# Optimization experiments

Hardware: AMD Instinct MI355X
Metric: run time of the kernel (lower is better)

Reference implementation:

```python
import math
import jax, jax.numpy as jnp
import numpy as np

B, T, HIDDEN = 2, 2048, 1024
H, HKV, D = 16, 16, 64


def _rope_tables(T, D):
    inv_freq = 1.0 / (10000.0 ** (jnp.arange(0, D, 2, dtype=jnp.float32) / D))
    t = jnp.arange(T, dtype=jnp.float32)
    freqs = jnp.outer(t, inv_freq)               # [T, D/2]
    emb = jnp.concatenate([freqs, freqs], axis=-1)  # [T, D]
    return jnp.cos(emb), jnp.sin(emb)


def setup_inputs() -> dict:
    key = jax.random.key(0)
    k1, k2, k3 = jax.random.split(key, 3)
    hidden_states = jax.random.normal(k1, (B, T, HIDDEN), dtype=jnp.float32)
    cos, sin = _rope_tables(T, D)
    # trunc-normal-ish init, std = 1/sqrt(fan_in)
    w_qkv = jax.random.normal(k2, ((H + 2 * HKV) * D, HIDDEN), dtype=jnp.float32) / math.sqrt(HIDDEN)
    w_o = jax.random.normal(k3, (HIDDEN, H * D), dtype=jnp.float32) / math.sqrt(H * D)
    return {"hidden_states": hidden_states, "cos": cos, "sin": sin, "w_qkv": w_qkv, "w_o": w_o}


def _rotate_half(x):
    x1, x2 = jnp.split(x, 2, axis=-1)
    return jnp.concatenate([-x2, x1], axis=-1)


def reference(hidden_states, cos, sin, w_qkv, w_o):
    b, t, _ = hidden_states.shape
    # fused QKV projection: [B,T,(H+2*HKV)*D]
    qkv = jnp.einsum('bti,oi->bto', hidden_states, w_qkv)
    qkv = qkv.reshape(b, t, H + 2 * HKV, D)
    q = qkv[:, :, :H]                    # [B,T,H,D]
    k = qkv[:, :, H:H + HKV]             # [B,T,HKV,D]
    v = qkv[:, :, H + HKV:]              # [B,T,HKV,D]
    # inline RoPE; cos/sin broadcast over heads
    c = cos[:, None, :]
    s = sin[:, None, :]
    q = q * c + _rotate_half(q) * s
    k = k * c + _rotate_half(k) * s
    scale = 1.0 / math.sqrt(D)
    attn_scores = jnp.einsum('bthd,bThd->bhtT', q, k) * scale  # [B,H,T,T]
    mask = jnp.tril(jnp.ones((t, t), dtype=bool))
    attn_scores = jnp.where(mask[None, None, :, :], attn_scores, -1e9)
    attn = jax.nn.softmax(attn_scores, axis=-1)
    context = jnp.einsum('bhtT,bThd->bthd', attn, v).reshape(b, t, H * D)
    return jnp.einsum('bti,oi->bto', context, w_o)
```

## Files before the change

kernel.cpp:

```cpp
#include <hip/hip_runtime.h>

typedef __bf16 bf16_t;
typedef __bf16 bf16x4 __attribute__((ext_vector_type(4)));
typedef __bf16 bf16x8 __attribute__((ext_vector_type(8)));
typedef float f32x4 __attribute__((ext_vector_type(4)));
typedef unsigned int u32x2 __attribute__((ext_vector_type(2)));
typedef unsigned long long u64;

#define MFMA16(a, b, c) __builtin_amdgcn_mfma_f32_16x16x32_bf16((a), (b), (c), 0, 0, 0)

#define LDG2LDS16(g, l)                                                        \
    __builtin_amdgcn_global_load_lds(                                          \
        (const __attribute__((address_space(1))) void*)(g),                    \
        (__attribute__((address_space(3))) void*)(l), 16, 0, 0)

#if __has_builtin(__builtin_amdgcn_exp2f)
#define EXP2(x) __builtin_amdgcn_exp2f(x)
#else
#define EXP2(x) exp2f(x)
#endif

__device__ inline bf16x8 load8(const float* p) {
    const f32x4 a = *(const f32x4*)p;
    const f32x4 b = *(const f32x4*)(p + 4);
    bf16x8 r;
#pragma unroll
    for (int i = 0; i < 4; i++) { r[i] = (bf16_t)a[i]; r[4 + i] = (bf16_t)b[i]; }
    return r;
}

__device__ inline u32x2 as2(bf16x4 v) {
    u32x2 r;
    __builtin_memcpy(&r, &v, 8);
    return r;
}

__device__ inline bf16x4 shfl4(bf16x4 v, int src) {
    u64 x;
    __builtin_memcpy(&x, &v, 8);
    x = __shfl(x, src, 64);
    bf16x4 r;
    __builtin_memcpy(&r, &x, 8);
    return r;
}

__global__ __launch_bounds__(256) void convert_kernel(const float* __restrict__ hs,
                                                      const float* __restrict__ wqkv,
                                                      const float* __restrict__ wo,
                                                      bf16_t* __restrict__ outb) {
    const size_t c = ((size_t)blockIdx.x * 256 + threadIdx.x) * 8;
    const float* src;
    size_t off;
    if (c < 4194304) { src = hs; off = c; }
    else if (c < 7340032) { src = wqkv; off = c - 4194304; }
    else { src = wo; off = c - 7340032; }
    *(bf16x8*)(outb + c) = load8(src + off);
}


template <int MODE, int NDIM, int BM>
__global__ __launch_bounds__(256) void gemm_bt(const bf16_t* __restrict__ A,
                                               const bf16_t* __restrict__ B,
                                               float* __restrict__ outp,
                                               bf16_t* __restrict__ q_ws,
                                               bf16_t* __restrict__ k_ws,
                                               bf16_t* __restrict__ v_ws,
                                               const float* __restrict__ cosb,
                                               const float* __restrict__ sinb) {
    constexpr int K = 1024;
    constexpr int IM = BM / 32;
    __shared__ __align__(16) bf16_t As[BM * 32];
    __shared__ __align__(16) bf16_t Bs[128 * 32];

    const int tid = threadIdx.x;
    const int w = tid >> 6;
    const int lane = tid & 63;
    const int lr = lane & 15;
    const int quad = lane >> 4;
    const int m0 = blockIdx.y * BM;
    const int n0 = blockIdx.x * 128;
    const int wm = (w & 1) * (BM / 2);
    const int wn = (w >> 1) * 64;

    const int srow = tid >> 2;
    const int skk = (((tid & 3) ^ ((tid >> 3) & 3)) * 8);
    const bf16_t* gA0 = A + (size_t)(m0 + srow) * K + skk;
    const bf16_t* gA1 = gA0 + (size_t)64 * K;
    const bf16_t* gB0 = B + (size_t)(n0 + srow) * K + skk;
    const bf16_t* gB1 = gB0 + (size_t)64 * K;
    bf16_t* lA0 = As + w * 512;
    bf16_t* lA1 = As + 2048 + w * 512;
    bf16_t* lB0 = Bs + w * 512;
    bf16_t* lB1 = Bs + 2048 + w * 512;

    const int qsw = (quad ^ ((lr >> 1) & 3)) * 8;

    f32x4 acc[IM][4] = {};

    for (int k0 = 0; k0 < K; k0 += 32) {
        LDG2LDS16(gA0 + k0, lA0);
        if constexpr (BM == 128) LDG2LDS16(gA1 + k0, lA1);
        LDG2LDS16(gB0 + k0, lB0);
        LDG2LDS16(gB1 + k0, lB1);
        __syncthreads();

        bf16x8 af[IM], bfm[4];
#pragma unroll
        for (int im = 0; im < IM; im++)
            af[im] = *(const bf16x8*)&As[(wm + im * 16 + lr) * 32 + qsw];
#pragma unroll
        for (int in = 0; in < 4; in++)
            bfm[in] = *(const bf16x8*)&Bs[(wn + in * 16 + lr) * 32 + qsw];
#pragma unroll
        for (int im = 0; im < IM; im++)
#pragma unroll
            for (int in = 0; in < 4; in++)
                acc[im][in] = MFMA16(af[im], bfm[in], acc[im][in]);
        __syncthreads();
    }

    if constexpr (MODE == 0) {
#pragma unroll
        for (int im = 0; im < IM; im++)
#pragma unroll
            for (int in = 0; in < 4; in++)
#pragma unroll
                for (int r = 0; r < 4; r++) {
                    const int m = m0 + wm + im * 16 + quad * 4 + r;
                    const int n = n0 + wn + in * 16 + lr;
                    outp[(size_t)m * NDIM + n] = acc[im][in][r];
                }
    } else {
        const int j = (n0 + wn) >> 6;
        if (j < 32) {
            const bool isq = (j < 16);
            const float qs = 0.125f * 1.44269504089f;
#pragma unroll
            for (int im = 0; im < IM; im++) {
#pragma unroll
                for (int r = 0; r < 4; r++) {
                    const int m = m0 + wm + im * 16 + quad * 4 + r;
                    const int b = m >> 11;
                    const int t = m & 2047;
#pragma unroll
                    for (int in = 0; in < 2; in++) {
                        const int d = in * 16 + lr;
                        const float x1 = acc[im][in][r];
                        const float x2 = acc[im][in + 2][r];
                        const float c = cosb[t * 64 + d];
                        const float s = sinb[t * 64 + d];
                        float y1 = x1 * c - x2 * s;
                        float y2 = x2 * c + x1 * s;
                        if (isq) {
                            y1 *= qs; y2 *= qs;
                            const size_t base =
                                ((size_t)(b * 16 + j) * 2048 + t) * 64 + d;
                            q_ws[base] = (bf16_t)y1;
                            q_ws[base + 32] = (bf16_t)y2;
                        } else {
                            const int bh = b * 16 + (j - 16);
                            const size_t off =
                                ((size_t)(bh * 128 + (t >> 4)) * 2) * 512 +
                                ((t & 15) + (d >> 3) * 16) * 8 + (d & 7);
                            k_ws[off] = (bf16_t)y1;
                            k_ws[off + 512] = (bf16_t)y2;
                        }
                    }
                }
            }
        } else {
#pragma unroll
            for (int im = 0; im < IM; im++)
#pragma unroll
                for (int in = 0; in < 4; in++)
#pragma unroll
                    for (int r = 0; r < 4; r++) {
                        const int m = m0 + wm + im * 16 + quad * 4 + r;
                        const int b = m >> 11;
                        const int t = m & 2047;
                        const int d = in * 16 + lr;
                        const int bh = b * 16 + (j - 32);
                        const size_t off =
                            ((size_t)(bh * 64 + (t >> 5)) * 4 + (d >> 4)) * 512 +
                            ((d & 15) + ((t & 31) >> 3) * 16) * 8 + (t & 7);
                        v_ws[off] = (bf16_t)acc[im][in][r];
                    }
        }
    }
}

__global__ __launch_bounds__(256) void attn_kernel(const bf16_t* __restrict__ q_ws,
                                                   const bf16_t* __restrict__ k_ws,
                                                   const bf16_t* __restrict__ v_ws,
                                                   bf16_t* __restrict__ ctx) {
    __shared__ __align__(16) bf16_t Ks[2][4096];
    __shared__ __align__(16) bf16_t Vs[2][4096];

    const int tid = threadIdx.x;
    const int w = tid >> 6;
    const int lane = tid & 63;
    const int lr = lane & 15;
    const int quad = lane >> 4;
    const int bh = blockIdx.x & 31;
    const int g = blockIdx.x >> 5;
    const int qt = (g & 1) ? (g >> 1) : (31 - (g >> 1));
    const int b = bh >> 4;
    const int hd = bh & 15;

    const bf16_t* kws = k_ws + (size_t)bh * 131072;
    const bf16_t* vws = v_ws + (size_t)bh * 131072;
    const int soff = w * 512 + lane * 8;
    const int lo8 = lane * 8;

#define ASTAGE(kb, buf)                                                        \
    {                                                                          \
        LDG2LDS16(kws + (size_t)(kb) * 4096 + soff, &Ks[buf][w * 512]);        \
        LDG2LDS16(kws + (size_t)(kb) * 4096 + 2048 + soff,                     \
                  &Ks[buf][2048 + w * 512]);                                   \
        LDG2LDS16(vws + (size_t)(kb) * 4096 + soff, &Vs[buf][w * 512]);        \
        LDG2LDS16(vws + (size_t)(kb) * 4096 + 2048 + soff,                     \
                  &Vs[buf][2048 + w * 512]);                                   \
    }

    const int trow = qt * 64 + w * 16;
    const int query = trow + lr;

    const bf16_t* qb = q_ws + ((size_t)bh * 2048 + trow + lr) * 64 + quad * 8;
    const bf16x8 qlo = *(const bf16x8*)qb;
    const bf16x8 qhi = *(const bf16x8*)(qb + 32);

    f32x4 o[4] = {};
    float lrun = 0.0f;

    ASTAGE(0, 0);
    asm volatile("s_waitcnt vmcnt(0)" ::: "memory");
    __builtin_amdgcn_s_barrier();
    asm volatile("" ::: "memory");

    for (int kb = 0; kb <= qt; kb++) {
        const int buf = kb & 1;
        if (kb < qt) ASTAGE(kb + 1, buf ^ 1);

        f32x4 s[4];
#pragma unroll
        for (int n = 0; n < 4; n++) {
            const bf16x8 k0 = *(const bf16x8*)&Ks[buf][(2 * n) * 512 + lo8];
            const bf16x8 k1 = *(const bf16x8*)&Ks[buf][(2 * n + 1) * 512 + lo8];
            const f32x4 z = {};
            s[n] = MFMA16(k0, qlo, z);
            s[n] = MFMA16(k1, qhi, s[n]);
        }

        const int u0 = kb * 64;
        if (kb == qt) {
#pragma unroll
            for (int n = 0; n < 4; n++)
#pragma unroll
                for (int r = 0; r < 4; r++)
                    if (u0 + n * 16 + quad * 4 + r > query) s[n][r] = -1e9f;
        }

        f32x4 p[4];
#pragma unroll
        for (int n = 0; n < 4; n++)
#pragma unroll
            for (int r = 0; r < 4; r++) p[n][r] = EXP2(s[n][r]);

        lrun += ((p[0][0] + p[0][1]) + (p[0][2] + p[0][3])) +
                ((p[1][0] + p[1][1]) + (p[1][2] + p[1][3])) +
                ((p[2][0] + p[2][1]) + (p[2][2] + p[2][3])) +
                ((p[3][0] + p[3][1]) + (p[3][2] + p[3][3]));

        bf16x4 pb[4];
#pragma unroll
        for (int n = 0; n < 4; n++)
#pragma unroll
            for (int r = 0; r < 4; r++) pb[n][r] = (bf16_t)p[n][r];

#pragma unroll
        for (int hh = 0; hh < 2; hh++) {
            bf16x8 pf;
#if __has_builtin(__builtin_amdgcn_permlane16_swap) && \
    __has_builtin(__builtin_amdgcn_permlane32_swap)
            const u32x2 P0 = as2(pb[2 * hh]);
            const u32x2 P1 = as2(pb[2 * hh + 1]);
            const u32x2 s1a = __builtin_amdgcn_permlane16_swap(P0[0], P0[1], false, false);
            const u32x2 s1b = __builtin_amdgcn_permlane16_swap(P1[0], P1[1], false, false);
            const u32x2 s2a = __builtin_amdgcn_permlane32_swap(s1a[0], s1b[0], false, false);
            const u32x2 s2b = __builtin_amdgcn_permlane32_swap(s1a[1], s1b[1], false, false);
            const u32x2 s3a = __builtin_amdgcn_permlane16_swap(s2a[0], s2a[1], false, false);
            const u32x2 s3b = __builtin_amdgcn_permlane16_swap(s2b[0], s2b[1], false, false);
            const unsigned pfd[4] = {s3a[0], s3a[1], s3b[0], s3b[1]};
            __builtin_memcpy(&pf, pfd, 16);
#else
            const int srcLow = ((quad & 1) << 5) + lr;
            const int srcHigh = srcLow + 16;
            const bool loSel = (quad < 2);
            const bf16x4 a0 = shfl4(pb[2 * hh], srcLow);
            const bf16x4 a1 = shfl4(pb[2 * hh + 1], srcLow);
            const bf16x4 b0 = shfl4(pb[2 * hh], srcHigh);
            const bf16x4 b1 = shfl4(pb[2 * hh + 1], srcHigh);
            const bf16x4 lo = loSel ? a0 : a1;
            const bf16x4 hi = loSel ? b0 : b1;
#pragma unroll
            for (int r = 0; r < 4; r++) { pf[r] = lo[r]; pf[4 + r] = hi[r]; }
#endif
#pragma unroll
            for (int n = 0; n < 4; n++) {
                const bf16x8 vvf =
                    *(const bf16x8*)&Vs[buf][(hh * 4 + n) * 512 + lo8];
                o[n] = MFMA16(vvf, pf, o[n]);
            }
        }

        asm volatile("s_waitcnt lgkmcnt(0) vmcnt(0)" ::: "memory");
        __builtin_amdgcn_s_barrier();
        asm volatile("" ::: "memory");
    }

    lrun += __shfl_xor(lrun, 16);
    lrun += __shfl_xor(lrun, 32);

    const float inv = 1.0f / fmaxf(lrun, 1e-30f);
    const size_t base = ((size_t)b * 2048 + query) * 1024 + hd * 64 + quad * 4;
#pragma unroll
    for (int n = 0; n < 4; n++) {
        bf16x4 ob;
#pragma unroll
        for (int r = 0; r < 4; r++) ob[r] = (bf16_t)(o[n][r] * inv);
        *(bf16x4*)&ctx[base + n * 16] = ob;
    }
#undef ASTAGE
}

extern "C" void kernel_launch(void* const* d_in, const int* in_sizes, int n_in,
                              void* d_out, int out_size, void* d_ws, size_t ws_size,
                              hipStream_t stream) {
    const float* hs = (const float*)d_in[0];
    const float* cosb = (const float*)d_in[1];
    const float* sinb = (const float*)d_in[2];
    const float* wqkv = (const float*)d_in[3];
    const float* wo = (const float*)d_in[4];
    float* out = (float*)d_out;

    char* ws = (char*)d_ws;
    bf16_t* hs_b = (bf16_t*)(ws);
    bf16_t* wqkv_b = hs_b + 4194304;
    bf16_t* wo_b = hs_b + 7340032;
    bf16_t* q_ws = (bf16_t*)(ws + (size_t)(16u << 20));
    bf16_t* k_ws = (bf16_t*)(ws + (size_t)(24u << 20));
    bf16_t* v_ws = (bf16_t*)(ws + (size_t)(32u << 20));
    bf16_t* ctx = (bf16_t*)(ws);

    const dim3 blk(256);

    convert_kernel<<<dim3(4096), blk, 0, stream>>>(hs, wqkv, wo, hs_b);

    gemm_bt<1, 3072, 128><<<dim3(24, 32), blk, 0, stream>>>(
        hs_b, wqkv_b, nullptr, q_ws, k_ws, v_ws, cosb, sinb);

    attn_kernel<<<dim3(1024), blk, 0, stream>>>(q_ws, k_ws, v_ws, ctx);

    gemm_bt<0, 1024, 64><<<dim3(8, 64), blk, 0, stream>>>(
        ctx, wo_b, out, nullptr, nullptr, nullptr, nullptr, nullptr);
}
```

Before: 176.1 us.

## Pair causal query tiles per 512-thread block and compute row sums via MFMA

The attention kernel now uses 512-thread blocks, each handling two query tiles (qt and 31-qt), so every block does the same total causal work and shares the K/V LDS stages. The first four waves stage K and the other four stage V. The softmax row-sum is moved from scalar adds plus cross-lane shuffles to an extra MFMA against a ones vector, and exp values go straight to bf16. Waves on the short tile sit idle at barriers once their rows are done, and the denominator is now summed from bf16-rounded probabilities.

```diff
diff --git a/kernel.cpp b/kernel.cpp
--- a/kernel.cpp
+++ b/kernel.cpp
@@ -42,6 +42,36 @@
     bf16x4 r;
     __builtin_memcpy(&r, &x, 8);
     return r;
+}
+
+__device__ inline bf16x8 p2pf(bf16x4 pb0, bf16x4 pb1, int quad, int lr) {
+    bf16x8 pf;
+#if __has_builtin(__builtin_amdgcn_permlane16_swap) && \
+    __has_builtin(__builtin_amdgcn_permlane32_swap)
+    const u32x2 P0 = as2(pb0);
+    const u32x2 P1 = as2(pb1);
+    const u32x2 s1a = __builtin_amdgcn_permlane16_swap(P0[0], P0[1], false, false);
+    const u32x2 s1b = __builtin_amdgcn_permlane16_swap(P1[0], P1[1], false, false);
+    const u32x2 s2a = __builtin_amdgcn_permlane32_swap(s1a[0], s1b[0], false, false);
+    const u32x2 s2b = __builtin_amdgcn_permlane32_swap(s1a[1], s1b[1], false, false);
+    const u32x2 s3a = __builtin_amdgcn_permlane16_swap(s2a[0], s2a[1], false, false);
+    const u32x2 s3b = __builtin_amdgcn_permlane16_swap(s2b[0], s2b[1], false, false);
+    const unsigned pfd[4] = {s3a[0], s3a[1], s3b[0], s3b[1]};
+    __builtin_memcpy(&pf, pfd, 16);
+#else
+    const int srcLow = ((quad & 1) << 5) + lr;
+    const int srcHigh = srcLow + 16;
+    const bool loSel = (quad < 2);
+    const bf16x4 a0 = shfl4(pb0, srcLow);
+    const bf16x4 a1 = shfl4(pb1, srcLow);
+    const bf16x4 b0 = shfl4(pb0, srcHigh);
+    const bf16x4 b1 = shfl4(pb1, srcHigh);
+    const bf16x4 lo = loSel ? a0 : a1;
+    const bf16x4 hi = loSel ? b0 : b1;
+#pragma unroll
+    for (int r = 0; r < 4; r++) { pf[r] = lo[r]; pf[4 + r] = hi[r]; }
+#endif
+    return pf;
 }
 
 __global__ __launch_bounds__(256) void convert_kernel(const float* __restrict__ hs,
@@ -189,40 +219,51 @@
     }
 }
 
-__global__ __launch_bounds__(256) void attn_kernel(const bf16_t* __restrict__ q_ws,
-                                                   const bf16_t* __restrict__ k_ws,
-                                                   const bf16_t* __restrict__ v_ws,
-                                                   bf16_t* __restrict__ ctx) {
+__global__ __launch_bounds__(512, 4) void attn_kernel(const bf16_t* __restrict__ q_ws,
+                                                      const bf16_t* __restrict__ k_ws,
+                                                      const bf16_t* __restrict__ v_ws,
+                                                      bf16_t* __restrict__ ctx) {
     __shared__ __align__(16) bf16_t Ks[2][4096];
     __shared__ __align__(16) bf16_t Vs[2][4096];
 
     const int tid = threadIdx.x;
     const int w = tid >> 6;
+    const int wq = w & 3;
     const int lane = tid & 63;
     const int lr = lane & 15;
     const int quad = lane >> 4;
     const int bh = blockIdx.x & 31;
     const int g = blockIdx.x >> 5;
-    const int qt = (g & 1) ? (g >> 1) : (31 - (g >> 1));
+    const int pr = (g < 8) ? g : 23 - g;
+    const int qtA = pr;
+    const int qtB = 31 - pr;
+    const int qtw = (w < 4) ? qtA : qtB;
     const int b = bh >> 4;
     const int hd = bh & 15;
 
     const bf16_t* kws = k_ws + (size_t)bh * 131072;
     const bf16_t* vws = v_ws + (size_t)bh * 131072;
-    const int soff = w * 512 + lane * 8;
+    const int soff = wq * 512 + lane * 8;
     const int lo8 = lane * 8;
 
-#define ASTAGE(kb, buf)                                                        \
+    bf16x8 ones8;
+#pragma unroll
+    for (int i = 0; i < 8; i++) ones8[i] = (bf16_t)1.0f;
+
+#define ASTAGE(kb, bufi)                                                       \
     {                                                                          \
-        LDG2LDS16(kws + (size_t)(kb) * 4096 + soff, &Ks[buf][w * 512]);        \
-        LDG2LDS16(kws + (size_t)(kb) * 4096 + 2048 + soff,                     \
-                  &Ks[buf][2048 + w * 512]);                                   \
-        LDG2LDS16(vws + (size_t)(kb) * 4096 + soff, &Vs[buf][w * 512]);        \
-        LDG2LDS16(vws + (size_t)(kb) * 4096 + 2048 + soff,                     \
-                  &Vs[buf][2048 + w * 512]);                                   \
-    }
-
-    const int trow = qt * 64 + w * 16;
+        if (w < 4) {                                                           \
+            LDG2LDS16(kws + (size_t)(kb) * 4096 + soff, &Ks[bufi][wq * 512]);  \
+            LDG2LDS16(kws + (size_t)(kb) * 4096 + 2048 + soff,                 \
+                      &Ks[bufi][2048 + wq * 512]);                             \
+        } else {                                                               \
+            LDG2LDS16(vws + (size_t)(kb) * 4096 + soff, &Vs[bufi][wq * 512]);  \
+            LDG2LDS16(vws + (size_t)(kb) * 4096 + 2048 + soff,                 \
+                      &Vs[bufi][2048 + wq * 512]);                             \
+        }                                                                      \
+    }
+
+    const int trow = qtw * 64 + wq * 16;
     const int query = trow + lr;
 
     const bf16_t* qb = q_ws + ((size_t)bh * 2048 + trow + lr) * 64 + quad * 8;
@@ -230,86 +271,54 @@
     const bf16x8 qhi = *(const bf16x8*)(qb + 32);
 
     f32x4 o[4] = {};
-    float lrun = 0.0f;
+    f32x4 lacc = {};
 
     ASTAGE(0, 0);
     asm volatile("s_waitcnt vmcnt(0)" ::: "memory");
     __builtin_amdgcn_s_barrier();
     asm volatile("" ::: "memory");
 
-    for (int kb = 0; kb <= qt; kb++) {
-        const int buf = kb & 1;
-        if (kb < qt) ASTAGE(kb + 1, buf ^ 1);
-
-        f32x4 s[4];
-#pragma unroll
-        for (int n = 0; n < 4; n++) {
-            const bf16x8 k0 = *(const bf16x8*)&Ks[buf][(2 * n) * 512 + lo8];
-            const bf16x8 k1 = *(const bf16x8*)&Ks[buf][(2 * n + 1) * 512 + lo8];
-            const f32x4 z = {};
-            s[n] = MFMA16(k0, qlo, z);
-            s[n] = MFMA16(k1, qhi, s[n]);
-        }
-
-        const int u0 = kb * 64;
-        if (kb == qt) {
+    for (int kb = 0; kb <= qtB; kb++) {
+        const int bufi = kb & 1;
+        if (kb < qtB) ASTAGE(kb + 1, bufi ^ 1);
+
+        if (kb <= qtw) {
+            f32x4 s[4];
+#pragma unroll
+            for (int n = 0; n < 4; n++) {
+                const bf16x8 k0 = *(const bf16x8*)&Ks[bufi][(2 * n) * 512 + lo8];
+                const bf16x8 k1 =
+                    *(const bf16x8*)&Ks[bufi][(2 * n + 1) * 512 + lo8];
+                const f32x4 z = {};
+                s[n] = MFMA16(k0, qlo, z);
+                s[n] = MFMA16(k1, qhi, s[n]);
+            }
+
+            const int u0 = kb * 64;
+            if (kb == qtw) {
+#pragma unroll
+                for (int n = 0; n < 4; n++)
+#pragma unroll
+                    for (int r = 0; r < 4; r++)
+                        if (u0 + n * 16 + quad * 4 + r > query) s[n][r] = -1e9f;
+            }
+
+            bf16x4 pb[4];
 #pragma unroll
             for (int n = 0; n < 4; n++)
 #pragma unroll
-                for (int r = 0; r < 4; r++)
-                    if (u0 + n * 16 + quad * 4 + r > query) s[n][r] = -1e9f;
-        }
-
-        f32x4 p[4];
-#pragma unroll
-        for (int n = 0; n < 4; n++)
-#pragma unroll
-            for (int r = 0; r < 4; r++) p[n][r] = EXP2(s[n][r]);
-
-        lrun += ((p[0][0] + p[0][1]) + (p[0][2] + p[0][3])) +
-                ((p[1][0] + p[1][1]) + (p[1][2] + p[1][3])) +
-                ((p[2][0] + p[2][1]) + (p[2][2] + p[2][3])) +
-                ((p[3][0] + p[3][1]) + (p[3][2] + p[3][3]));
-
-        bf16x4 pb[4];
-#pragma unroll
-        for (int n = 0; n < 4; n++)
-#pragma unroll
-            for (int r = 0; r < 4; r++) pb[n][r] = (bf16_t)p[n][r];
-
-#pragma unroll
-        for (int hh = 0; hh < 2; hh++) {
-            bf16x8 pf;
-#if __has_builtin(__builtin_amdgcn_permlane16_swap) && \
-    __has_builtin(__builtin_amdgcn_permlane32_swap)
-            const u32x2 P0 = as2(pb[2 * hh]);
-            const u32x2 P1 = as2(pb[2 * hh + 1]);
-            const u32x2 s1a = __builtin_amdgcn_permlane16_swap(P0[0], P0[1], false, false);
-            const u32x2 s1b = __builtin_amdgcn_permlane16_swap(P1[0], P1[1], false, false);
-            const u32x2 s2a = __builtin_amdgcn_permlane32_swap(s1a[0], s1b[0], false, false);
-            const u32x2 s2b = __builtin_amdgcn_permlane32_swap(s1a[1], s1b[1], false, false);
-            const u32x2 s3a = __builtin_amdgcn_permlane16_swap(s2a[0], s2a[1], false, false);
-            const u32x2 s3b = __builtin_amdgcn_permlane16_swap(s2b[0], s2b[1], false, false);
-            const unsigned pfd[4] = {s3a[0], s3a[1], s3b[0], s3b[1]};
-            __builtin_memcpy(&pf, pfd, 16);
-#else
-            const int srcLow = ((quad & 1) << 5) + lr;
-            const int srcHigh = srcLow + 16;
-            const bool loSel = (quad < 2);
-            const bf16x4 a0 = shfl4(pb[2 * hh], srcLow);
-            const bf16x4 a1 = shfl4(pb[2 * hh + 1], srcLow);
-            const bf16x4 b0 = shfl4(pb[2 * hh], srcHigh);
-            const bf16x4 b1 = shfl4(pb[2 * hh + 1], srcHigh);
-            const bf16x4 lo = loSel ? a0 : a1;
-            const bf16x4 hi = loSel ? b0 : b1;
-#pragma unroll
-            for (int r = 0; r < 4; r++) { pf[r] = lo[r]; pf[4 + r] = hi[r]; }
-#endif
-#pragma unroll
-            for (int n = 0; n < 4; n++) {
-                const bf16x8 vvf =
-                    *(const bf16x8*)&Vs[buf][(hh * 4 + n) * 512 + lo8];
-                o[n] = MFMA16(vvf, pf, o[n]);
+                for (int r = 0; r < 4; r++) pb[n][r] = (bf16_t)EXP2(s[n][r]);
+
+#pragma unroll
+            for (int hh = 0; hh < 2; hh++) {
+                const bf16x8 pf = p2pf(pb[2 * hh], pb[2 * hh + 1], quad, lr);
+                lacc = MFMA16(ones8, pf, lacc);
+#pragma unroll
+                for (int n = 0; n < 4; n++) {
+                    const bf16x8 vvf =
+                        *(const bf16x8*)&Vs[bufi][(hh * 4 + n) * 512 + lo8];
+                    o[n] = MFMA16(vvf, pf, o[n]);
+                }
             }
         }
 
@@ -318,10 +327,7 @@
         asm volatile("" ::: "memory");
     }
 
-    lrun += __shfl_xor(lrun, 16);
-    lrun += __shfl_xor(lrun, 32);
-
-    const float inv = 1.0f / fmaxf(lrun, 1e-30f);
+    const float inv = 1.0f / fmaxf(lacc[0], 1e-30f);
     const size_t base = ((size_t)b * 2048 + query) * 1024 + hd * 64 + quad * 4;
 #pragma unroll
     for (int n = 0; n < 4; n++) {
@@ -359,7 +365,7 @@
     gemm_bt<1, 3072, 128><<<dim3(24, 32), blk, 0, stream>>>(
         hs_b, wqkv_b, nullptr, q_ws, k_ws, v_ws, cosb, sinb);
 
-    attn_kernel<<<dim3(1024), blk, 0, stream>>>(q_ws, k_ws, v_ws, ctx);
+    attn_kernel<<<dim3(512), dim3(512), 0, stream>>>(q_ws, k_ws, v_ws, ctx);
 
     gemm_bt<0, 1024, 64><<<dim3(8, 64), blk, 0, stream>>>(
         ctx, wo_b, out, nullptr, nullptr, nullptr, nullptr, nullptr);
```

New measurement: 164.8 us. 1.07x faster.
